# Kernel optimization log

Measured on AMD Instinct MI355X. Metric: run time of the kernel, lower is better.

## Reference

```python
import jax, jax.numpy as jnp
import numpy as np
from jax import lax

STRIDE = 8
DIST = float(np.sqrt(2.0) / 2.0)


def _conv_bn_leaky(x, w, gamma, beta):
    # 3x3 conv, stride 1, pad 1 (SAME), then batch-norm (training-mode batch stats) + leaky relu 0.1
    y = lax.conv_general_dilated(x, w, (1, 1), 'SAME',
                                 dimension_numbers=('NCHW', 'OIHW', 'NCHW'))
    m = y.mean(axis=(0, 2, 3))
    v = y.var(axis=(0, 2, 3))
    scale = (gamma / jnp.sqrt(v + 1e-5))[None, :, None, None]
    y = (y - m[None, :, None, None]) * scale + beta[None, :, None, None]
    return jnp.where(y > 0, y, 0.1 * y)


def _decode(p, offset_vertex):
    # p: [B,S,S,10], offset_vertex: [B,S,S,22]
    B, S = p.shape[0], p.shape[1]
    st = jnp.asarray(STRIDE, p.dtype)
    gx = jnp.tile(jnp.arange(S, dtype=p.dtype)[None, :], (S, 1))  # x varies along last dim
    gy = gx.T
    gX = gx[None, :, :, None]  # [1,S,S,1]
    gY = gy[None, :, :, None]

    raw_l, raw_s, raw_r, raw_conf = p[..., 0:4], p[..., 4:8], p[..., 8:9], p[..., 9:10]
    l = raw_l ** 2 * st
    xmin = gX * st + st / 2 - l[..., 3:4]
    ymin = gY * st + st / 2 - l[..., 0:1]
    xmax = gX * st + st / 2 + l[..., 1:2]
    ymax = gY * st + st / 2 + l[..., 2:3]
    w = l[..., 1:2] + l[..., 3:4]
    h = l[..., 0:1] + l[..., 2:3]
    xc = (xmax + xmin) / 2
    yc = (ymax + ymin) / 2
    xywh = jnp.concatenate([xc, yc, w, h], axis=-1)

    r = jax.nn.sigmoid(raw_r)
    maskr = jnp.where(r > 0.9, jnp.zeros_like(r), jnp.ones_like(r))
    s = jax.nn.sigmoid(raw_s) * maskr
    conf = jax.nn.sigmoid(raw_conf)
    bbox = jnp.concatenate([xywh, s, r, l, conf], axis=-1)  # [B,S,S,14]

    x1 = xmin + s[..., 0:1] * w
    x7 = xmax - s[..., 2:3] * w
    y5 = ymin + s[..., 1:2] * h
    y3 = ymax - s[..., 3:4] * h
    x_obb = (x1 + x7) / 2
    y_obb = (y5 + y3) / 2

    off_y_t = ymin / st + 1 - gY
    off_y_b = ymax / st - 1 - gY
    off_x_l = xmin / st + 1 - gX
    off_x_r = xmax / st - 1 - gX
    off_y3 = y3 / st - gY
    off_y4 = jnp.zeros_like(y_obb)
    off_y5 = y5 / st - gY
    off_x1 = x1 / st - gX
    off_x4 = jnp.zeros_like(x_obb)
    off_x7 = x7 / st - gX

    off = jax.nn.sigmoid(offset_vertex)
    dc_off = off[..., 4:]  # 18 channels
    eps = jnp.ceil(0.01 * w)

    xp0 = jnp.where(x1 < xmin + eps, x1, xmin + off[..., 0:1] * (x1 - xmin))
    yp0 = jnp.where(x1 < xmin + eps, ymin + off[..., 0:1] * (y3 - ymin),
                    (y3 - ymin) / (xmin - x1 + 1e-8) * (xp0 - x1) + ymin)
    xp2 = jnp.where(x1 > xmax - eps, x1, xmax - off[..., 1:2] * (xmax - x1))
    yp2 = jnp.where(x1 > xmax - eps, ymin + off[..., 1:2] * (y5 - ymin),
                    (y5 - ymin) / (xmax - x1 + 1e-8) * (xp2 - x1) + ymin)
    xp6 = jnp.where(x7 < xmin + eps, x7, xmin + off[..., 2:3] * (x7 - xmin))
    yp6 = jnp.where(x7 < xmin + eps, ymax - off[..., 2:3] * (ymax - y3),
                    (y3 - ymax) / (xmin - x7 + 1e-8) * (xp6 - x7) + ymax)
    xp8 = jnp.where(x7 > xmax - eps, x7, xmax - off[..., 3:4] * (xmax - x7))
    yp8 = jnp.where(x7 > xmax - eps, ymax - off[..., 3:4] * (ymax - y5),
                    (y5 - ymax) / (xmax - x7 + 1e-8) * (xp8 - x7) + ymax)

    off_y_0 = yp0 / st + 1 - gY
    off_x_0 = xp0 / st + 1 - gX
    off_y_2 = yp2 / st + 1 - gY
    off_x_2 = xp2 / st - 1 - gX
    off_y_6 = yp6 / st - 1 - gY
    off_x_6 = xp6 / st + 1 - gX
    off_y_8 = yp8 / st - 1 - gY
    off_x_8 = xp8 / st - 1 - gX

    offsets_loc = jnp.concatenate(
        [off_y_0, off_x_0, off_y_t, off_x1, off_y_2, off_x_2, off_y3, off_x_l,
         off_y4, off_x4, off_y5, off_x_r, off_y_6, off_x_6, off_y_b, off_x7,
         off_y_8, off_x_8], axis=-1)
    offsets_loc = jnp.transpose(offsets_loc, (0, 3, 1, 2))  # [B,18,S,S]

    width = lax.stop_gradient(jnp.sqrt((x1 - xmax) ** 2 + (ymin - y5) ** 2)
                              + jnp.sqrt((xmin - x7) ** 2 + (y3 - ymax) ** 2)) / 2
    height = lax.stop_gradient(jnp.sqrt((xmin - x1) ** 2 + (y3 - ymin) ** 2)
                               + jnp.sqrt((x7 - xmax) ** 2 + (ymax - y5) ** 2)) / 2
    angle = (jnp.arctan((y5 - ymin) / (xmax - x1 + 1e-4))
             + jnp.arctan((ymax - y3) / (x7 - xmin + 1e-4))) / 2

    xd = lax.stop_gradient(x_obb) - width / 2 + dc_off[..., 9:18] * width   # [B,S,S,9]
    yd = lax.stop_gradient(y_obb) - height / 2 + dc_off[..., 0:9] * height  # [B,S,S,9]
    ca, sa = jnp.cos(angle), jnp.sin(angle)
    xd0 = ca * (xd - x_obb) - sa * (yd - y_obb) + x_obb
    # faithful to the nested torch.where (outer branch uses the unclipped xd0)
    xd_ = jnp.where(jnp.where(xd0 >= xmin, xd0, xmin) <= xmax, xd0, xmax)
    yd0 = sa * (xd - x_obb) + ca * (yd - y_obb) + y_obb
    yd_ = jnp.where(jnp.where(yd0 >= ymin, yd0, ymin) <= ymax, yd0, ymax)

    dy = jnp.array([DIST, 1.0, DIST, 0.0, 0.0, 0.0, -DIST, -1.0, -DIST], p.dtype)
    dx = jnp.array([DIST, 0.0, -DIST, 1.0, 0.0, -1.0, DIST, 0.0, -DIST], p.dtype)
    dc_y = yd_ / st + dy - gY  # [B,S,S,9]
    dc_x = xd_ / st + dx - gX
    # interleave y0,x0,y1,x1,... -> 18 channels
    offsets_cls = jnp.stack([dc_y, dc_x], axis=-1).reshape(B, S, S, 18)
    offsets_cls = jnp.transpose(offsets_cls, (0, 3, 1, 2))

    coor_dc = jnp.concatenate([xd_, yd_], axis=-1).reshape(-1, 18)
    return bbox, offsets_loc, offsets_cls, coor_dc


def reference(input1, w_conv, bn_gamma, bn_beta, w_loc, b_loc, w_mask, b_mask):
    B, C, S, _ = input1.shape
    gx = jnp.tile(jnp.arange(S, dtype=input1.dtype)[None, :], (S, 1))
    gy = gx.T
    grid = jnp.broadcast_to(jnp.stack([gx, gy])[None], (B, 2, S, S))  # channel0=x, channel1=y
    x = jnp.concatenate([input1, grid], axis=1)
    conv = _conv_bn_leaky(x, w_conv, bn_gamma, bn_beta)  # [B, 2C, S, S]

    out1 = jnp.einsum('bchw,oc->bohw', conv, w_loc) + b_loc[None, :, None, None]
    cm = jnp.einsum('bchw,oc->bohw', conv, w_mask) + b_mask[None, :, None, None]

    mask_loc = jax.nn.sigmoid(cm[:, 0:9])
    mask_cls = jax.nn.sigmoid(cm[:, 9:18])
    offset_vertex = jnp.transpose(cm[:, 18:40], (0, 2, 3, 1))  # [B,S,S,22]
    weight_c8 = jax.nn.softmax(cm[:, 40:48], axis=1)

    p = jnp.transpose(out1, (0, 2, 3, 1))  # [B,S,S,10]
    bbox, offsets_loc, offsets_cls, offsets_d = _decode(p, offset_vertex)
    return (p, bbox, offsets_loc, offsets_cls, mask_loc, mask_cls, weight_c8, offsets_d)


def setup_inputs() -> dict:
    key = jax.random.key(0)
    ks = jax.random.split(key, 5)
    B, C, S = 16, 256, 64
    return {
        'input1': jax.random.normal(ks[0], (B, C, S, S), dtype=jnp.float32),
        'w_conv': jax.random.normal(ks[1], (2 * C, C + 2, 3, 3), dtype=jnp.float32) * 0.02,
        'bn_gamma': jnp.ones((2 * C,), jnp.float32),
        'bn_beta': jnp.zeros((2 * C,), jnp.float32),
        'w_loc': jax.random.normal(ks[2], (10, 2 * C), dtype=jnp.float32) * 0.02,
        'b_loc': jnp.zeros((10,), jnp.float32),
        'w_mask': jax.random.normal(ks[3], (48, 2 * C), dtype=jnp.float32) * 0.02,
        'b_mask': jnp.zeros((48,), jnp.float32),
    }
```

## Files before the change

### kernel.cpp

```cpp
#include <hip/hip_runtime.h>

typedef __attribute__((ext_vector_type(4))) float f32x4;
typedef __attribute__((ext_vector_type(4))) unsigned int u32x4;
typedef __attribute__((ext_vector_type(8))) unsigned short u16x8;
typedef __attribute__((ext_vector_type(8))) __bf16 bf16x8;

#define DEVFN static __device__ __forceinline__

DEVFN unsigned short f2b(float f) {
  unsigned u = __builtin_bit_cast(unsigned, f);
  u += 0x7fffu + ((u >> 16) & 1u);
  return (unsigned short)(u >> 16);
}
DEVFN float b2f(unsigned short h) {
  unsigned u = ((unsigned)h) << 16;
  return __builtin_bit_cast(float, u);
}
DEVFN float sigf(float x) { return 1.0f / (1.0f + __expf(-x)); }

#define CS 264
#define KPAD 2432
#define NTILE 38

#define XP_BYTES (16ull*66*66*CS*2)
#define WT_BYTES (512ull*KPAD*2)
#define W2_BYTES (64ull*512*2)
#define CV_BYTES (65536ull*512*2)
#define PS_BYTES (512ull*256*2*4)
#define XP_OFF 0ull
#define WT_OFF (XP_OFF + XP_BYTES)
#define W2_OFF (WT_OFF + WT_BYTES)
#define CV_OFF (W2_OFF + W2_BYTES)
#define PS_OFF (CV_OFF + CV_BYTES)
#define SB_OFF (PS_OFF + PS_BYTES)

#define GLOAD16(gp, lp) __builtin_amdgcn_global_load_lds( \
    (__attribute__((address_space(1))) void*)(gp),        \
    (__attribute__((address_space(3))) void*)(lp), 16, 0, 0)

#define BAR()  do { __builtin_amdgcn_s_barrier(); __builtin_amdgcn_sched_barrier(0); } while (0)
#define WLG0() do { asm volatile("s_waitcnt lgkmcnt(0)" ::: "memory"); __builtin_amdgcn_sched_barrier(0); } while (0)

__global__ void k_prep(const float* __restrict__ wc, const float* __restrict__ wl,
                       const float* __restrict__ wm, unsigned short* __restrict__ xp,
                       unsigned short* __restrict__ wt, unsigned short* __restrict__ w2) {
  int bid = blockIdx.x, tid = threadIdx.x;
  if (bid < 537) {
    int idx = bid * 256 + tid;
    if (idx >= 137280) return;
    int cell_i = idx / 33, u = idx - cell_i * 33;
    int b = cell_i / 260, r = cell_i - b * 260;
    int y, x;
    if (r < 66) { y = 0; x = r; }
    else if (r < 132) { y = 65; x = r - 66; }
    else if (r < 196) { y = r - 131; x = 0; }
    else { y = r - 195; x = 65; }
    int cell = (b * 66 + y) * 66 + x;
    *(u32x4*)((unsigned char*)xp + (size_t)cell * (CS * 2) + u * 16) = (u32x4){0u, 0u, 0u, 0u};
  } else if (bid < 793) {
    int pid = (bid - 537) * 256 + tid;
    int b = pid >> 12, pi = pid & 4095, y = pi >> 6, x = pi & 63;
    u16x8 v0 = (u16x8){0, 0, 0, 0, 0, 0, 0, 0};
    v0[0] = f2b((float)x); v0[1] = f2b((float)y);
    *(u16x8*)(xp + ((size_t)((b * 66 + y + 1) * 66 + x + 1)) * CS + 256) = v0;
  } else if (bid < 5657) {
    int idx = (bid - 793) * 256 + tid;
    int o = idx / KPAD, k = idx - o * KPAD;
    int dy = k / 800, t = k - dy * 800;
    int dx = t / CS, ci = t - dx * CS;
    float v = (dy < 3 && dx < 3 && ci < 258) ? wc[(size_t)(o * 258 + ci) * 9 + dy * 3 + dx] : 0.f;
    wt[idx] = f2b(v);
  } else {
    int idx = (bid - 5657) * 256 + tid;
    int o = idx >> 9, k = idx & 511;
    float v = 0.f;
    if (o < 10) v = wl[o * 512 + k];
    else if (o < 58) v = wm[(o - 10) * 512 + k];
    w2[idx] = f2b(v);
  }
}

__global__ void k_pack_in(const float* __restrict__ in1, unsigned short* __restrict__ xp) {
  __shared__ float lt[32][65];
  int tid = threadIdx.x;
  int bid = blockIdx.x;
  int cg = bid & 7, y = (bid >> 3) & 63, b = bid >> 9;
  int x = tid & 63, cr = tid >> 6;
#pragma unroll
  for (int i = 0; i < 8; ++i) {
    int cl = i * 4 + cr;
    lt[cl][x] = in1[(((size_t)(b * 256 + cg * 32 + cl) * 64 + y) * 64) + x];
  }
  __syncthreads();
  int xx = tid >> 2, ch = tid & 3;
  u16x8 v;
#pragma unroll
  for (int j = 0; j < 8; ++j) v[j] = f2b(lt[ch * 8 + j][xx]);
  size_t base = ((size_t)((b * 66 + y + 1) * 66 + xx + 1)) * CS + cg * 32 + ch * 8;
  *(u16x8*)(xp + base) = v;
}

__global__ __launch_bounds__(512, 2) void k_conv8(const unsigned short* __restrict__ xp,
                                                  const unsigned short* __restrict__ wt,
                                                  unsigned short* __restrict__ cv,
                                                  float* __restrict__ ps) {
  extern __shared__ char smem[];
  int tid = threadIdx.x, lane = tid & 63, wv = tid >> 6;
  int wm = wv >> 2, wn = wv & 3;
  int bid = blockIdx.x;
  int xcd = bid & 7, j = bid >> 3;
  int nt = j & 1;
  int mt = xcd * 32 + (j >> 1);
  int n0 = nt * 256;
  int pix0 = mt * 256;
  int b = pix0 >> 12, pi0 = pix0 & 4095;

  int srow = tid >> 3;
  int ug = (tid & 7) ^ (srow & 7);
  unsigned cellB[4], oB[4];
#pragma unroll
  for (int jj = 0; jj < 4; ++jj) {
    int pi = pi0 + srow + 64 * jj;
    int yy = pi >> 6, xx = pi & 63;
    cellB[jj] = (unsigned)((b * 66 + yy) * 66 + xx) * (CS * 2);
    oB[jj] = (unsigned)(n0 + srow + 64 * jj) * (KPAD * 2);
  }

  auto stageA = [&](int tau, int h) {
    int buf = tau & 1;
    unsigned k = (unsigned)tau * 64u + (unsigned)ug * 8u;
    unsigned dy = k / 800u;
    unsigned t = k - dy * 800u;
    unsigned off = dy * (66u * CS * 2u) + t * 2u;
    const unsigned char* g = (const unsigned char*)xp;
    char* l = smem + buf * 65536 + h * 16384;
    GLOAD16(g + cellB[h * 2] + off, l + tid * 16);
    GLOAD16(g + cellB[h * 2 + 1] + off, l + 8192 + tid * 16);
  };
  auto stageB = [&](int tau, int h) {
    int buf = tau & 1;
    unsigned k2 = ((unsigned)tau * 64u + (unsigned)ug * 8u) * 2u;
    const unsigned char* g = (const unsigned char*)wt;
    char* l = smem + buf * 65536 + 32768 + h * 16384;
    GLOAD16(g + oB[h * 2] + k2, l + tid * 16);
    GLOAD16(g + oB[h * 2 + 1] + k2, l + 8192 + tid * 16);
  };

  unsigned aoffb[8], boffb[4];
#pragma unroll
  for (int mf = 0; mf < 8; ++mf) aoffb[mf] = (unsigned)(wm * 128 + mf * 16 + (lane & 15)) * 128u;
#pragma unroll
  for (int nf = 0; nf < 4; ++nf) boffb[nf] = 32768u + (unsigned)(wn * 64 + nf * 16 + (lane & 15)) * 128u;
  int ko = (lane >> 4) & 3, xm = lane & 7;
  unsigned un[2];
#pragma unroll
  for (int kk = 0; kk < 2; ++kk) un[kk] = (unsigned)(((kk * 4 + ko) ^ xm) * 16);

  f32x4 acc[8][4];
#pragma unroll
  for (int i = 0; i < 8; ++i)
#pragma unroll
    for (int jj = 0; jj < 4; ++jj) acc[i][jj] = (f32x4){0.f, 0.f, 0.f, 0.f};

  stageB(0, 0); stageB(0, 1); stageA(0, 0); stageA(0, 1); stageB(1, 0); stageB(1, 1);
  asm volatile("s_waitcnt vmcnt(4)" ::: "memory");
  __builtin_amdgcn_sched_barrier(0);
  BAR();

  bf16x8 af[4][2], bfr[4][2];
#define MM(mi, ni, kk, ab) acc[(ab) + (mi)][(ni)] = \
    __builtin_amdgcn_mfma_f32_16x16x32_bf16(af[(mi)][(kk)], bfr[(ni)][(kk)], acc[(ab) + (mi)][(ni)], 0, 0, 0)

#pragma unroll 1
  for (int tau = 0; tau < NTILE; ++tau) {
    bool sA = tau < NTILE - 1, sB = tau < NTILE - 2;
    const char* base = smem + (tau & 1) * 65536;
    auto rdA = [&](int s, int kk, int hi) { af[s][kk] = *(const bf16x8*)(base + aoffb[hi * 4 + s] + un[kk]); };
    auto rdB = [&](int s, int kk) { bfr[s][kk] = *(const bf16x8*)(base + boffb[s] + un[kk]); };

    rdA(0, 0, 0); rdA(1, 0, 0); rdA(2, 0, 0); rdA(3, 0, 0);
    rdB(0, 0); rdB(1, 0); rdB(2, 0); rdB(3, 0);
    WLG0();
    __builtin_amdgcn_s_setprio(1);
    MM(0, 0, 0, 0); MM(0, 1, 0, 0); rdA(0, 1, 0);
    MM(0, 2, 0, 0); MM(0, 3, 0, 0); rdA(1, 1, 0);
    MM(1, 0, 0, 0); MM(1, 1, 0, 0); rdA(2, 1, 0);
    MM(1, 2, 0, 0); MM(1, 3, 0, 0); rdA(3, 1, 0);
    MM(2, 0, 0, 0); MM(2, 1, 0, 0); rdB(0, 1);
    MM(2, 2, 0, 0); MM(2, 3, 0, 0); rdB(1, 1);
    MM(3, 0, 0, 0); MM(3, 1, 0, 0); rdB(2, 1);
    MM(3, 2, 0, 0); MM(3, 3, 0, 0); rdB(3, 1);
    __builtin_amdgcn_s_setprio(0);
    if (sA) stageA(tau + 1, 0);
    BAR();

    WLG0();
    __builtin_amdgcn_s_setprio(1);
    MM(0, 0, 1, 0); MM(0, 1, 1, 0); MM(0, 2, 1, 0); MM(0, 3, 1, 0); rdA(0, 0, 1);
    MM(1, 0, 1, 0); MM(1, 1, 1, 0); MM(1, 2, 1, 0); MM(1, 3, 1, 0); rdA(1, 0, 1);
    MM(2, 0, 1, 0); MM(2, 1, 1, 0); MM(2, 2, 1, 0); MM(2, 3, 1, 0); rdA(2, 0, 1);
    MM(3, 0, 1, 0); MM(3, 1, 1, 0); MM(3, 2, 1, 0); MM(3, 3, 1, 0); rdA(3, 0, 1);
    __builtin_amdgcn_s_setprio(0);
    if (sA) stageA(tau + 1, 1);
    BAR();

    WLG0();
    __builtin_amdgcn_s_setprio(1);
    MM(0, 0, 0, 4); MM(0, 1, 0, 4); MM(0, 2, 0, 4); MM(0, 3, 0, 4); rdA(0, 1, 1);
    MM(1, 0, 0, 4); MM(1, 1, 0, 4); MM(1, 2, 0, 4); MM(1, 3, 0, 4); rdA(1, 1, 1);
    MM(2, 0, 0, 4); MM(2, 1, 0, 4); MM(2, 2, 0, 4); MM(2, 3, 0, 4); rdA(2, 1, 1);
    MM(3, 0, 0, 4); MM(3, 1, 0, 4); MM(3, 2, 0, 4); MM(3, 3, 0, 4); rdA(3, 1, 1);
    __builtin_amdgcn_s_setprio(0);
    if (sB) stageB(tau + 2, 0);
    BAR();

    WLG0();
    __builtin_amdgcn_s_setprio(1);
    MM(0, 0, 1, 4); MM(0, 1, 1, 4); MM(0, 2, 1, 4); MM(0, 3, 1, 4);
    MM(1, 0, 1, 4); MM(1, 1, 1, 4); MM(1, 2, 1, 4); MM(1, 3, 1, 4);
    MM(2, 0, 1, 4); MM(2, 1, 1, 4); MM(2, 2, 1, 4); MM(2, 3, 1, 4);
    MM(3, 0, 1, 4); MM(3, 1, 1, 4); MM(3, 2, 1, 4); MM(3, 3, 1, 4);
    __builtin_amdgcn_s_setprio(0);
    if (sB) stageB(tau + 2, 1);
    if (tau < NTILE - 2) { asm volatile("s_waitcnt vmcnt(4)" ::: "memory"); __builtin_amdgcn_sched_barrier(0); }
    else if (tau == NTILE - 2) { asm volatile("s_waitcnt vmcnt(0)" ::: "memory"); __builtin_amdgcn_sched_barrier(0); }
    BAR();
  }
#undef MM

  unsigned short* l16 = (unsigned short*)smem;
#pragma unroll
  for (int mf = 0; mf < 8; ++mf)
#pragma unroll
    for (int nf = 0; nf < 4; ++nf)
#pragma unroll
      for (int r = 0; r < 4; ++r) {
        int row = wm * 128 + mf * 16 + (lane >> 4) * 4 + r;
        int col = wn * 64 + nf * 16 + (lane & 15);
        int colx = col ^ (((row >> 2) & 3) << 3);
        l16[row * 256 + colx] = f2b(acc[mf][nf][r]);
      }
  __syncthreads();
#pragma unroll
  for (int i = 0; i < 16; ++i) {
    int q = tid + 512 * i;
    int prow = q >> 5, c16 = q & 31;
    int c16g = c16 ^ ((prow >> 2) & 3);
    *(u16x8*)(cv + ((size_t)(pix0 + prow) * 512 + n0 + c16g * 8)) = *(const u16x8*)(l16 + q * 8);
  }
  __syncthreads();

  float* lf = (float*)smem;
  float sv[4], qv[4];
#pragma unroll
  for (int nf = 0; nf < 4; ++nf) {
    float s = 0.f, q = 0.f;
#pragma unroll
    for (int mf = 0; mf < 8; ++mf)
#pragma unroll
      for (int r = 0; r < 4; ++r) { float v = acc[mf][nf][r]; s += v; q += v * v; }
    s += __shfl_xor(s, 16); s += __shfl_xor(s, 32);
    q += __shfl_xor(q, 16); q += __shfl_xor(q, 32);
    sv[nf] = s; qv[nf] = q;
  }
  if (lane < 16) {
#pragma unroll
    for (int nf = 0; nf < 4; ++nf) {
      int ch = wn * 64 + nf * 16 + lane;
      lf[wm * 256 + ch] = sv[nf];
      lf[512 + wm * 256 + ch] = qv[nf];
    }
  }
  __syncthreads();
  if (tid < 256) {
    float S = lf[tid] + lf[256 + tid];
    float Q = lf[512 + tid] + lf[768 + tid];
    ((float2*)ps)[(size_t)(n0 + tid) * 256 + mt] = make_float2(S, Q);
  }
}

__global__ void k_bnfinal(const float* __restrict__ ps, const float* __restrict__ gamma,
                          const float* __restrict__ beta, float* __restrict__ sb) {
  int c = blockIdx.x * 32 + (threadIdx.x >> 3);
  int sl = threadIdx.x & 7;
  const float2* p2 = (const float2*)ps + (size_t)c * 256 + sl * 32;
  float s = 0.f, q = 0.f;
#pragma unroll 8
  for (int i = 0; i < 32; ++i) { float2 v = p2[i]; s += v.x; q += v.y; }
  s += __shfl_xor(s, 1); s += __shfl_xor(s, 2); s += __shfl_xor(s, 4);
  q += __shfl_xor(q, 1); q += __shfl_xor(q, 2); q += __shfl_xor(q, 4);
  if (sl == 0) {
    float mean = s * (1.0f / 65536.0f);
    float var = q * (1.0f / 65536.0f) - mean * mean;
    float sc = gamma[c] / sqrtf(var + 1e-5f);
    sb[c] = sc;
    sb[512 + c] = beta[c] - mean * sc;
  }
}

__global__ __launch_bounds__(256) void k_head(const unsigned short* __restrict__ cv,
                                              const unsigned short* __restrict__ w2,
                                              const float* __restrict__ bl,
                                              const float* __restrict__ bm,
                                              const float* __restrict__ sb,
                                              float* __restrict__ out) {
  __shared__ float lo[256][59];
  __shared__ float sS[512], sBb[512];
  int tid = threadIdx.x, lane = tid & 63, wv = tid >> 6;
  int pix0 = blockIdx.x * 256;
  sS[tid] = sb[tid]; sS[256 + tid] = sb[256 + tid];
  sBb[tid] = sb[512 + tid]; sBb[256 + tid] = sb[768 + tid];
  __syncthreads();

  f32x4 acc[4][4];
#pragma unroll
  for (int mf = 0; mf < 4; ++mf)
#pragma unroll
    for (int nf = 0; nf < 4; ++nf) acc[mf][nf] = (f32x4){0.f, 0.f, 0.f, 0.f};
  int ko = lane >> 4;

  for (int k0 = 0; k0 < 512; k0 += 32) {
    int c0 = k0 + ko * 8;
    f32x4 sc0 = *(const f32x4*)&sS[c0], sc1 = *(const f32x4*)&sS[c0 + 4];
    f32x4 bo0 = *(const f32x4*)&sBb[c0], bo1 = *(const f32x4*)&sBb[c0 + 4];
    bf16x8 a[4], bg[4];
#pragma unroll
    for (int f = 0; f < 4; ++f) {
      bg[f] = *(const bf16x8*)(w2 + (size_t)(f * 16 + (lane & 15)) * 512 + c0);
      u16x8 raw = *(const u16x8*)(cv + (size_t)(pix0 + wv * 64 + f * 16 + (lane & 15)) * 512 + c0);
      u16x8 av;
#pragma unroll
      for (int jj = 0; jj < 4; ++jj) {
        float v = b2f(raw[jj]) * sc0[jj] + bo0[jj];
        v = (v > 0.f) ? v : 0.1f * v;
        av[jj] = f2b(v);
      }
#pragma unroll
      for (int jj = 0; jj < 4; ++jj) {
        float v = b2f(raw[4 + jj]) * sc1[jj] + bo1[jj];
        v = (v > 0.f) ? v : 0.1f * v;
        av[4 + jj] = f2b(v);
      }
      a[f] = __builtin_bit_cast(bf16x8, av);
    }
#pragma unroll
    for (int mf = 0; mf < 4; ++mf)
#pragma unroll
      for (int nf = 0; nf < 4; ++nf)
        acc[mf][nf] = __builtin_amdgcn_mfma_f32_16x16x32_bf16(a[mf], bg[nf], acc[mf][nf], 0, 0, 0);
  }

  float bias[4]; int colv[4];
#pragma unroll
  for (int nf = 0; nf < 4; ++nf) {
    int col = nf * 16 + (lane & 15);
    colv[nf] = col;
    bias[nf] = (col < 10) ? bl[col] : ((col < 58) ? bm[col - 10] : 0.f);
  }
#pragma unroll
  for (int mf = 0; mf < 4; ++mf)
#pragma unroll
    for (int nf = 0; nf < 4; ++nf)
#pragma unroll
      for (int r = 0; r < 4; ++r) {
        int row = wv * 64 + mf * 16 + (lane >> 4) * 4 + r;
        if (colv[nf] < 58) lo[row][colv[nf]] = acc[mf][nf][r] + bias[nf];
      }
  __syncthreads();

  int pix = pix0 + tid;
  int b = pix >> 12, pi = pix & 4095;
  int yi = pi >> 6, xi = pi & 63;
  float X = (float)xi, Y = (float)yi;
  const float* O = lo[tid];

  float* outP = out;
  float* outB = out + 655360;
  float* outOL = out + 1572864;
  float* outOC = out + 2752512;
  float* outML = out + 3932160;
  float* outMC = out + 4521984;
  float* outWC = out + 5111808;
  float* outOD = out + 5636096;

  float pr[10];
#pragma unroll
  for (int i = 0; i < 10; ++i) { pr[i] = O[i]; outP[(size_t)pix * 10 + i] = pr[i]; }
  const float st = 8.f, ist = 0.125f;
  float l0 = pr[0] * pr[0] * st, l1 = pr[1] * pr[1] * st;
  float l2 = pr[2] * pr[2] * st, l3 = pr[3] * pr[3] * st;
  float cx = X * st + 4.f, cy = Y * st + 4.f;
  float xmin = cx - l3, ymin = cy - l0, xmax = cx + l1, ymax = cy + l2;
  float w = l1 + l3, h = l0 + l2;
  float xc = 0.5f * (xmax + xmin), yc = 0.5f * (ymax + ymin);
  float r = sigf(pr[8]);
  float maskr = (r > 0.9f) ? 0.f : 1.f;
  float s0 = sigf(pr[4]) * maskr, s1 = sigf(pr[5]) * maskr;
  float s2 = sigf(pr[6]) * maskr, s3 = sigf(pr[7]) * maskr;
  float conf = sigf(pr[9]);
  {
    size_t bo = (size_t)pix * 14;
    outB[bo + 0] = xc; outB[bo + 1] = yc; outB[bo + 2] = w; outB[bo + 3] = h;
    outB[bo + 4] = s0; outB[bo + 5] = s1; outB[bo + 6] = s2; outB[bo + 7] = s3;
    outB[bo + 8] = r;  outB[bo + 9] = l0; outB[bo + 10] = l1; outB[bo + 11] = l2;
    outB[bo + 12] = l3; outB[bo + 13] = conf;
  }
  float x1 = xmin + s0 * w, x7 = xmax - s2 * w;
  float y5 = ymin + s1 * h, y3 = ymax - s3 * h;
  float xob = 0.5f * (x1 + x7), yob = 0.5f * (y5 + y3);
  float ov[22];
#pragma unroll
  for (int jj = 0; jj < 22; ++jj) ov[jj] = sigf(O[28 + jj]);
  float eps = ceilf(0.01f * w);
  bool c0 = x1 < xmin + eps;
  float xp0 = c0 ? x1 : xmin + ov[0] * (x1 - xmin);
  float yp0 = c0 ? ymin + ov[0] * (y3 - ymin)
                 : (y3 - ymin) / (xmin - x1 + 1e-8f) * (xp0 - x1) + ymin;
  bool c2 = x1 > xmax - eps;
  float xp2 = c2 ? x1 : xmax - ov[1] * (xmax - x1);
  float yp2 = c2 ? ymin + ov[1] * (y5 - ymin)
                 : (y5 - ymin) / (xmax - x1 + 1e-8f) * (xp2 - x1) + ymin;
  bool c6 = x7 < xmin + eps;
  float xp6 = c6 ? x7 : xmin + ov[2] * (x7 - xmin);
  float yp6 = c6 ? ymax - ov[2] * (ymax - y3)
                 : (y3 - ymax) / (xmin - x7 + 1e-8f) * (xp6 - x7) + ymax;
  bool c8c = x7 > xmax - eps;
  float xp8 = c8c ? x7 : xmax - ov[3] * (xmax - x7);
  float yp8 = c8c ? ymax - ov[3] * (ymax - y5)
                  : (y5 - ymax) / (xmax - x7 + 1e-8f) * (xp8 - x7) + ymax;

  size_t olb = ((size_t)b * 18) * 4096 + pi;
  outOL[olb + 0 * 4096] = yp0 * ist + 1.f - Y;
  outOL[olb + 1 * 4096] = xp0 * ist + 1.f - X;
  outOL[olb + 2 * 4096] = ymin * ist + 1.f - Y;
  outOL[olb + 3 * 4096] = x1 * ist - X;
  outOL[olb + 4 * 4096] = yp2 * ist + 1.f - Y;
  outOL[olb + 5 * 4096] = xp2 * ist - 1.f - X;
  outOL[olb + 6 * 4096] = y3 * ist - Y;
  outOL[olb + 7 * 4096] = xmin * ist + 1.f - X;
  outOL[olb + 8 * 4096] = 0.f;
  outOL[olb + 9 * 4096] = 0.f;
  outOL[olb + 10 * 4096] = y5 * ist - Y;
  outOL[olb + 11 * 4096] = xmax * ist - 1.f - X;
  outOL[olb + 12 * 4096] = yp6 * ist - 1.f - Y;
  outOL[olb + 13 * 4096] = xp6 * ist + 1.f - X;
  outOL[olb + 14 * 4096] = ymax * ist - 1.f - Y;
  outOL[olb + 15 * 4096] = x7 * ist - X;
  outOL[olb + 16 * 4096] = yp8 * ist - 1.f - Y;
  outOL[olb + 17 * 4096] = xp8 * ist - 1.f - X;

  float A1 = x1 - xmax, B1 = ymin - y5, A2 = xmin - x7, B2 = y3 - ymax;
  float width = 0.5f * (sqrtf(A1 * A1 + B1 * B1) + sqrtf(A2 * A2 + B2 * B2));
  float C1 = xmin - x1, D1 = y3 - ymin, C2 = x7 - xmax, D2 = ymax - y5;
  float height = 0.5f * (sqrtf(C1 * C1 + D1 * D1) + sqrtf(C2 * C2 + D2 * D2));
  float ang = 0.5f * (atanf((y5 - ymin) / (xmax - x1 + 1e-4f)) +
                      atanf((ymax - y3) / (x7 - xmin + 1e-4f)));
  float ca = cosf(ang), sa = sinf(ang);
  const float DD = 0.70710678118654752f;
  const float dyc[9] = {DD, 1.f, DD, 0.f, 0.f, 0.f, -DD, -1.f, -DD};
  const float dxc[9] = {DD, 0.f, -DD, 1.f, 0.f, -1.f, DD, 0.f, -DD};
  size_t ocb = ((size_t)b * 18) * 4096 + pi;
  size_t odb = (size_t)pix * 18;
#pragma unroll
  for (int k = 0; k < 9; ++k) {
    float xd = xob - 0.5f * width + ov[13 + k] * width;
    float yd = yob - 0.5f * height + ov[4 + k] * height;
    float ddx = xd - xob, ddy = yd - yob;
    float xd0 = ca * ddx - sa * ddy + xob;
    float xdc = fminf(fmaxf(xd0, xmin), xmax);
    float yd0 = sa * ddx + ca * ddy + yob;
    float ydc = fminf(fmaxf(yd0, ymin), ymax);
    outOC[ocb + (size_t)(2 * k) * 4096] = ydc * ist + dyc[k] - Y;
    outOC[ocb + (size_t)(2 * k + 1) * 4096] = xdc * ist + dxc[k] - X;
    outOD[odb + k] = xdc;
    outOD[odb + 9 + k] = ydc;
  }
  size_t mlb = ((size_t)b * 9) * 4096 + pi;
#pragma unroll
  for (int k = 0; k < 9; ++k) outML[mlb + (size_t)k * 4096] = sigf(O[10 + k]);
#pragma unroll
  for (int k = 0; k < 9; ++k) outMC[mlb + (size_t)k * 4096] = sigf(O[19 + k]);
  float v8[8], mx = -1e30f;
#pragma unroll
  for (int k = 0; k < 8; ++k) { v8[k] = O[50 + k]; mx = fmaxf(mx, v8[k]); }
  float sm = 0.f;
#pragma unroll
  for (int k = 0; k < 8; ++k) { v8[k] = __expf(v8[k] - mx); sm += v8[k]; }
  float inv = 1.f / sm;
  size_t wcb = ((size_t)b * 8) * 4096 + pi;
#pragma unroll
  for (int k = 0; k < 8; ++k) outWC[wcb + (size_t)k * 4096] = v8[k] * inv;
}

extern "C" void kernel_launch(void* const* d_in, const int* in_sizes, int n_in,
                              void* d_out, int out_size, void* d_ws, size_t ws_size,
                              hipStream_t stream) {
  const float* in1 = (const float*)d_in[0];
  const float* wconv = (const float*)d_in[1];
  const float* gamma = (const float*)d_in[2];
  const float* beta = (const float*)d_in[3];
  const float* wloc = (const float*)d_in[4];
  const float* bloc = (const float*)d_in[5];
  const float* wmask = (const float*)d_in[6];
  const float* bmask = (const float*)d_in[7];
  unsigned char* ws = (unsigned char*)d_ws;
  unsigned short* xp = (unsigned short*)(ws + XP_OFF);
  unsigned short* wt = (unsigned short*)(ws + WT_OFF);
  unsigned short* w2 = (unsigned short*)(ws + W2_OFF);
  unsigned short* cv = (unsigned short*)(ws + CV_OFF);
  float* ps = (float*)(ws + PS_OFF);
  float* sb = (float*)(ws + SB_OFF);
  float* out = (float*)d_out;

  (void)hipFuncSetAttribute(reinterpret_cast<const void*>(k_conv8),
                            hipFuncAttributeMaxDynamicSharedMemorySize, 131072);

  k_prep<<<dim3(5785), dim3(256), 0, stream>>>(wconv, wloc, wmask, xp, wt, w2);
  k_pack_in<<<dim3(8192), dim3(256), 0, stream>>>(in1, xp);
  k_conv8<<<dim3(512), dim3(512), 131072, stream>>>(xp, wt, cv, ps);
  k_bnfinal<<<dim3(16), dim3(256), 0, stream>>>(ps, gamma, beta, sb);
  k_head<<<dim3(256), dim3(256), 0, stream>>>(cv, w2, bloc, bmask, sb, out);
}
```

Baseline: 211.6 us.

## Load conv weight fragments directly to registers from pre-swizzled global layout

The prep kernel now writes the conv weights in a fragment-ordered layout, so each lane can load its MFMA B operands straight from global memory into registers. The weights are double-buffered in registers one tile ahead, which removes weight staging through LDS and halves LDS use per stage. The main loop is restructured to have one barrier per K-tile instead of four. In exchange, every wave fetches its own weight fragments from global or L2 memory, register pressure rises, and each tile waits on vmcnt(0).

```diff
diff --git a/kernel.cpp b/kernel.cpp
--- a/kernel.cpp
+++ b/kernel.cpp
@@ -43,7 +43,7 @@
 
 __global__ void k_prep(const float* __restrict__ wc, const float* __restrict__ wl,
                        const float* __restrict__ wm, unsigned short* __restrict__ xp,
-                       unsigned short* __restrict__ wt, unsigned short* __restrict__ w2) {
+                       unsigned short* __restrict__ wt2, unsigned short* __restrict__ w2) {
   int bid = blockIdx.x, tid = threadIdx.x;
   if (bid < 537) {
     int idx = bid * 256 + tid;
@@ -69,7 +69,10 @@
     int dy = k / 800, t = k - dy * 800;
     int dx = t / CS, ci = t - dx * CS;
     float v = (dy < 3 && dx < 3 && ci < 258) ? wc[(size_t)(o * 258 + ci) * 9 + dy * 3 + dx] : 0.f;
-    wt[idx] = f2b(v);
+    int ntv = o >> 8, o2 = o & 255, wn = o2 >> 6, o3 = o2 & 63, nf = o3 >> 4, r = o3 & 15;
+    int tau = k >> 6, k2 = k & 63, kk = k2 >> 5, k3 = k2 & 31, ko = k3 >> 3, e = k3 & 7;
+    size_t off = ((size_t)(((ntv * 38 + tau) * 4 + wn) * 8 + nf * 2 + kk)) * 512 + (ko * 16 + r) * 8 + e;
+    wt2[off] = f2b(v);
   } else {
     int idx = (bid - 5657) * 256 + tid;
     int o = idx >> 9, k = idx & 511;
@@ -101,7 +104,7 @@
 }
 
 __global__ __launch_bounds__(512, 2) void k_conv8(const unsigned short* __restrict__ xp,
-                                                  const unsigned short* __restrict__ wt,
+                                                  const unsigned short* __restrict__ wt2,
                                                   unsigned short* __restrict__ cv,
                                                   float* __restrict__ ps) {
   extern __shared__ char smem[];
@@ -117,13 +120,12 @@
 
   int srow = tid >> 3;
   int ug = (tid & 7) ^ (srow & 7);
-  unsigned cellB[4], oB[4];
+  unsigned cellB[4];
 #pragma unroll
   for (int jj = 0; jj < 4; ++jj) {
     int pi = pi0 + srow + 64 * jj;
     int yy = pi >> 6, xx = pi & 63;
     cellB[jj] = (unsigned)((b * 66 + yy) * 66 + xx) * (CS * 2);
-    oB[jj] = (unsigned)(n0 + srow + 64 * jj) * (KPAD * 2);
   }
 
   auto stageA = [&](int tau, int h) {
@@ -133,100 +135,163 @@
     unsigned t = k - dy * 800u;
     unsigned off = dy * (66u * CS * 2u) + t * 2u;
     const unsigned char* g = (const unsigned char*)xp;
-    char* l = smem + buf * 65536 + h * 16384;
+    char* l = smem + buf * 32768 + h * 16384;
     GLOAD16(g + cellB[h * 2] + off, l + tid * 16);
     GLOAD16(g + cellB[h * 2 + 1] + off, l + 8192 + tid * 16);
   };
-  auto stageB = [&](int tau, int h) {
-    int buf = tau & 1;
-    unsigned k2 = ((unsigned)tau * 64u + (unsigned)ug * 8u) * 2u;
-    const unsigned char* g = (const unsigned char*)wt;
-    char* l = smem + buf * 65536 + 32768 + h * 16384;
-    GLOAD16(g + oB[h * 2] + k2, l + tid * 16);
-    GLOAD16(g + oB[h * 2 + 1] + k2, l + 8192 + tid * 16);
-  };
-
-  unsigned aoffb[8], boffb[4];
+
+  unsigned aoffb[8];
 #pragma unroll
   for (int mf = 0; mf < 8; ++mf) aoffb[mf] = (unsigned)(wm * 128 + mf * 16 + (lane & 15)) * 128u;
-#pragma unroll
-  for (int nf = 0; nf < 4; ++nf) boffb[nf] = 32768u + (unsigned)(wn * 64 + nf * 16 + (lane & 15)) * 128u;
   int ko = (lane >> 4) & 3, xm = lane & 7;
   unsigned un[2];
 #pragma unroll
   for (int kk = 0; kk < 2; ++kk) un[kk] = (unsigned)(((kk * 4 + ko) ^ xm) * 16);
 
+  const char* wb = (const char*)wt2 + ((size_t)(nt * 38 * 4 + wn) * 8) * 1024 + (size_t)lane * 16;
+  const size_t WTAU = 4 * 8 * 1024;
+
   f32x4 acc[8][4];
 #pragma unroll
   for (int i = 0; i < 8; ++i)
 #pragma unroll
     for (int jj = 0; jj < 4; ++jj) acc[i][jj] = (f32x4){0.f, 0.f, 0.f, 0.f};
 
-  stageB(0, 0); stageB(0, 1); stageA(0, 0); stageA(0, 1); stageB(1, 0); stageB(1, 1);
-  asm volatile("s_waitcnt vmcnt(4)" ::: "memory");
+  bf16x8 af[4][2], bA[4][2], bB[4][2];
+
+  stageA(0, 0); stageA(0, 1);
+#pragma unroll
+  for (int nf = 0; nf < 4; ++nf) {
+    bA[nf][0] = *(const bf16x8*)(wb + (nf * 2 + 0) * 1024);
+    bA[nf][1] = *(const bf16x8*)(wb + (nf * 2 + 1) * 1024);
+  }
+  asm volatile("s_waitcnt vmcnt(0)" ::: "memory");
   __builtin_amdgcn_sched_barrier(0);
   BAR();
-
-  bf16x8 af[4][2], bfr[4][2];
-#define MM(mi, ni, kk, ab) acc[(ab) + (mi)][(ni)] = \
-    __builtin_amdgcn_mfma_f32_16x16x32_bf16(af[(mi)][(kk)], bfr[(ni)][(kk)], acc[(ab) + (mi)][(ni)], 0, 0, 0)
+  {
+    const char* base0 = smem;
+#pragma unroll
+    for (int s = 0; s < 4; ++s) af[s][0] = *(const bf16x8*)(base0 + aoffb[s] + un[0]);
+  }
+
+#define MMX(mi, ni, kk, ab, BC) acc[(ab) + (mi)][(ni)] = \
+    __builtin_amdgcn_mfma_f32_16x16x32_bf16(af[(mi)][(kk)], BC[(ni)][(kk)], acc[(ab) + (mi)][(ni)], 0, 0, 0)
+
+#define TILE_STEADY(tau, BC, BN)                                                        \
+  {                                                                                     \
+    const char* base = smem + ((tau) & 1) * 32768;                                      \
+    const char* nbase = smem + (((tau) + 1) & 1) * 32768;                               \
+    const char* wbn = wb + (size_t)((tau) + 1) * WTAU;                                  \
+                                                                    \
+    BN[0][0] = *(const bf16x8*)(wbn + 0 * 1024);                                        \
+    BN[0][1] = *(const bf16x8*)(wbn + 1 * 1024);                                        \
+    BN[1][0] = *(const bf16x8*)(wbn + 2 * 1024);                                        \
+    BN[1][1] = *(const bf16x8*)(wbn + 3 * 1024);                                        \
+    BN[2][0] = *(const bf16x8*)(wbn + 4 * 1024);                                        \
+    BN[2][1] = *(const bf16x8*)(wbn + 5 * 1024);                                        \
+    BN[3][0] = *(const bf16x8*)(wbn + 6 * 1024);                                        \
+    BN[3][1] = *(const bf16x8*)(wbn + 7 * 1024);                                        \
+                                                        \
+    WLG0();                                                                             \
+    __builtin_amdgcn_s_setprio(1);                                                      \
+    MMX(0, 0, 0, 0, BC); MMX(0, 1, 0, 0, BC); MMX(0, 2, 0, 0, BC); MMX(0, 3, 0, 0, BC); \
+    af[0][1] = *(const bf16x8*)(base + aoffb[0] + un[1]);                               \
+    MMX(1, 0, 0, 0, BC); MMX(1, 1, 0, 0, BC); MMX(1, 2, 0, 0, BC); MMX(1, 3, 0, 0, BC); \
+    af[1][1] = *(const bf16x8*)(base + aoffb[1] + un[1]);                               \
+    MMX(2, 0, 0, 0, BC); MMX(2, 1, 0, 0, BC); MMX(2, 2, 0, 0, BC); MMX(2, 3, 0, 0, BC); \
+    af[2][1] = *(const bf16x8*)(base + aoffb[2] + un[1]);                               \
+    MMX(3, 0, 0, 0, BC); MMX(3, 1, 0, 0, BC); MMX(3, 2, 0, 0, BC); MMX(3, 3, 0, 0, BC); \
+    af[3][1] = *(const bf16x8*)(base + aoffb[3] + un[1]);                               \
+    __builtin_amdgcn_s_setprio(0);                                                      \
+    stageA((tau) + 1, 0);                                                               \
+                                                        \
+    WLG0();                                                                             \
+    __builtin_amdgcn_s_setprio(1);                                                      \
+    MMX(0, 0, 1, 0, BC); MMX(0, 1, 1, 0, BC); MMX(0, 2, 1, 0, BC); MMX(0, 3, 1, 0, BC); \
+    af[0][0] = *(const bf16x8*)(base + aoffb[4] + un[0]);                               \
+    MMX(1, 0, 1, 0, BC); MMX(1, 1, 1, 0, BC); MMX(1, 2, 1, 0, BC); MMX(1, 3, 1, 0, BC); \
+    af[1][0] = *(const bf16x8*)(base + aoffb[5] + un[0]);                               \
+    MMX(2, 0, 1, 0, BC); MMX(2, 1, 1, 0, BC); MMX(2, 2, 1, 0, BC); MMX(2, 3, 1, 0, BC); \
+    af[2][0] = *(const bf16x8*)(base + aoffb[6] + un[0]);                               \
+    MMX(3, 0, 1, 0, BC); MMX(3, 1, 1, 0, BC); MMX(3, 2, 1, 0, BC); MMX(3, 3, 1, 0, BC); \
+    af[3][0] = *(const bf16x8*)(base + aoffb[7] + un[0]);                               \
+    __builtin_amdgcn_s_setprio(0);                                                      \
+    stageA((tau) + 1, 1);                                                               \
+                         \
+    WLG0();                                                                             \
+    __builtin_amdgcn_s_setprio(1);                                                      \
+    MMX(0, 0, 0, 4, BC); MMX(0, 1, 0, 4, BC); MMX(0, 2, 0, 4, BC); MMX(0, 3, 0, 4, BC); \
+    af[0][1] = *(const bf16x8*)(base + aoffb[4] + un[1]);                               \
+    MMX(1, 0, 0, 4, BC); MMX(1, 1, 0, 4, BC); MMX(1, 2, 0, 4, BC); MMX(1, 3, 0, 4, BC); \
+    af[1][1] = *(const bf16x8*)(base + aoffb[5] + un[1]);                               \
+    MMX(2, 0, 0, 4, BC); MMX(2, 1, 0, 4, BC); MMX(2, 2, 0, 4, BC); MMX(2, 3, 0, 4, BC); \
+    af[2][1] = *(const bf16x8*)(base + aoffb[6] + un[1]);                               \
+    MMX(3, 0, 0, 4, BC); MMX(3, 1, 0, 4, BC); MMX(3, 2, 0, 4, BC); MMX(3, 3, 0, 4, BC); \
+    af[3][1] = *(const bf16x8*)(base + aoffb[7] + un[1]);                               \
+    __builtin_amdgcn_s_setprio(0);                                                      \
+    asm volatile("s_waitcnt vmcnt(0) lgkmcnt(0)" ::: "memory");                         \
+    __builtin_amdgcn_sched_barrier(0);                                                  \
+    BAR();                                                                              \
+                                                   \
+    __builtin_amdgcn_s_setprio(1);                                                      \
+    MMX(0, 0, 1, 4, BC); MMX(0, 1, 1, 4, BC); MMX(0, 2, 1, 4, BC); MMX(0, 3, 1, 4, BC); \
+    af[0][0] = *(const bf16x8*)(nbase + aoffb[0] + un[0]);                              \
+    MMX(1, 0, 1, 4, BC); MMX(1, 1, 1, 4, BC); MMX(1, 2, 1, 4, BC); MMX(1, 3, 1, 4, BC); \
+    af[1][0] = *(const bf16x8*)(nbase + aoffb[1] + un[0]);                              \
+    MMX(2, 0, 1, 4, BC); MMX(2, 1, 1, 4, BC); MMX(2, 2, 1, 4, BC); MMX(2, 3, 1, 4, BC); \
+    af[2][0] = *(const bf16x8*)(nbase + aoffb[2] + un[0]);                              \
+    MMX(3, 0, 1, 4, BC); MMX(3, 1, 1, 4, BC); MMX(3, 2, 1, 4, BC); MMX(3, 3, 1, 4, BC); \
+    af[3][0] = *(const bf16x8*)(nbase + aoffb[3] + un[0]);                              \
+    __builtin_amdgcn_s_setprio(0);                                                      \
+  }
 
 #pragma unroll 1
-  for (int tau = 0; tau < NTILE; ++tau) {
-    bool sA = tau < NTILE - 1, sB = tau < NTILE - 2;
-    const char* base = smem + (tau & 1) * 65536;
-    auto rdA = [&](int s, int kk, int hi) { af[s][kk] = *(const bf16x8*)(base + aoffb[hi * 4 + s] + un[kk]); };
-    auto rdB = [&](int s, int kk) { bfr[s][kk] = *(const bf16x8*)(base + boffb[s] + un[kk]); };
-
-    rdA(0, 0, 0); rdA(1, 0, 0); rdA(2, 0, 0); rdA(3, 0, 0);
-    rdB(0, 0); rdB(1, 0); rdB(2, 0); rdB(3, 0);
+  for (int t2 = 0; t2 < 18; ++t2) {
+    int tau = t2 * 2;
+    TILE_STEADY(tau, bA, bB);
+    TILE_STEADY(tau + 1, bB, bA);
+  }
+  TILE_STEADY(36, bA, bB);
+
+  {
+    const char* base = smem + 32768;
     WLG0();
-    __builtin_amdgcn_s_setprio(1);
-    MM(0, 0, 0, 0); MM(0, 1, 0, 0); rdA(0, 1, 0);
-    MM(0, 2, 0, 0); MM(0, 3, 0, 0); rdA(1, 1, 0);
-    MM(1, 0, 0, 0); MM(1, 1, 0, 0); rdA(2, 1, 0);
-    MM(1, 2, 0, 0); MM(1, 3, 0, 0); rdA(3, 1, 0);
-    MM(2, 0, 0, 0); MM(2, 1, 0, 0); rdB(0, 1);
-    MM(2, 2, 0, 0); MM(2, 3, 0, 0); rdB(1, 1);
-    MM(3, 0, 0, 0); MM(3, 1, 0, 0); rdB(2, 1);
-    MM(3, 2, 0, 0); MM(3, 3, 0, 0); rdB(3, 1);
-    __builtin_amdgcn_s_setprio(0);
-    if (sA) stageA(tau + 1, 0);
-    BAR();
-
+    MMX(0, 0, 0, 0, bB); MMX(0, 1, 0, 0, bB); MMX(0, 2, 0, 0, bB); MMX(0, 3, 0, 0, bB);
+    af[0][1] = *(const bf16x8*)(base + aoffb[0] + un[1]);
+    MMX(1, 0, 0, 0, bB); MMX(1, 1, 0, 0, bB); MMX(1, 2, 0, 0, bB); MMX(1, 3, 0, 0, bB);
+    af[1][1] = *(const bf16x8*)(base + aoffb[1] + un[1]);
+    MMX(2, 0, 0, 0, bB); MMX(2, 1, 0, 0, bB); MMX(2, 2, 0, 0, bB); MMX(2, 3, 0, 0, bB);
+    af[2][1] = *(const bf16x8*)(base + aoffb[2] + un[1]);
+    MMX(3, 0, 0, 0, bB); MMX(3, 1, 0, 0, bB); MMX(3, 2, 0, 0, bB); MMX(3, 3, 0, 0, bB);
+    af[3][1] = *(const bf16x8*)(base + aoffb[3] + un[1]);
     WLG0();
-    __builtin_amdgcn_s_setprio(1);
-    MM(0, 0, 1, 0); MM(0, 1, 1, 0); MM(0, 2, 1, 0); MM(0, 3, 1, 0); rdA(0, 0, 1);
-    MM(1, 0, 1, 0); MM(1, 1, 1, 0); MM(1, 2, 1, 0); MM(1, 3, 1, 0); rdA(1, 0, 1);
-    MM(2, 0, 1, 0); MM(2, 1, 1, 0); MM(2, 2, 1, 0); MM(2, 3, 1, 0); rdA(2, 0, 1);
-    MM(3, 0, 1, 0); MM(3, 1, 1, 0); MM(3, 2, 1, 0); MM(3, 3, 1, 0); rdA(3, 0, 1);
-    __builtin_amdgcn_s_setprio(0);
-    if (sA) stageA(tau + 1, 1);
-    BAR();
-
+    MMX(0, 0, 1, 0, bB); MMX(0, 1, 1, 0, bB); MMX(0, 2, 1, 0, bB); MMX(0, 3, 1, 0, bB);
+    af[0][0] = *(const bf16x8*)(base + aoffb[4] + un[0]);
+    MMX(1, 0, 1, 0, bB); MMX(1, 1, 1, 0, bB); MMX(1, 2, 1, 0, bB); MMX(1, 3, 1, 0, bB);
+    af[1][0] = *(const bf16x8*)(base + aoffb[5] + un[0]);
+    MMX(2, 0, 1, 0, bB); MMX(2, 1, 1, 0, bB); MMX(2, 2, 1, 0, bB); MMX(2, 3, 1, 0, bB);
+    af[2][0] = *(const bf16x8*)(base + aoffb[6] + un[0]);
+    MMX(3, 0, 1, 0, bB); MMX(3, 1, 1, 0, bB); MMX(3, 2, 1, 0, bB); MMX(3, 3, 1, 0, bB);
+    af[3][0] = *(const bf16x8*)(base + aoffb[7] + un[0]);
     WLG0();
-    __builtin_amdgcn_s_setprio(1);
-    MM(0, 0, 0, 4); MM(0, 1, 0, 4); MM(0, 2, 0, 4); MM(0, 3, 0, 4); rdA(0, 1, 1);
-    MM(1, 0, 0, 4); MM(1, 1, 0, 4); MM(1, 2, 0, 4); MM(1, 3, 0, 4); rdA(1, 1, 1);
-    MM(2, 0, 0, 4); MM(2, 1, 0, 4); MM(2, 2, 0, 4); MM(2, 3, 0, 4); rdA(2, 1, 1);
-    MM(3, 0, 0, 4); MM(3, 1, 0, 4); MM(3, 2, 0, 4); MM(3, 3, 0, 4); rdA(3, 1, 1);
-    __builtin_amdgcn_s_setprio(0);
-    if (sB) stageB(tau + 2, 0);
-    BAR();
-
+    MMX(0, 0, 0, 4, bB); MMX(0, 1, 0, 4, bB); MMX(0, 2, 0, 4, bB); MMX(0, 3, 0, 4, bB);
+    af[0][1] = *(const bf16x8*)(base + aoffb[4] + un[1]);
+    MMX(1, 0, 0, 4, bB); MMX(1, 1, 0, 4, bB); MMX(1, 2, 0, 4, bB); MMX(1, 3, 0, 4, bB);
+    af[1][1] = *(const bf16x8*)(base + aoffb[5] + un[1]);
+    MMX(2, 0, 0, 4, bB); MMX(2, 1, 0, 4, bB); MMX(2, 2, 0, 4, bB); MMX(2, 3, 0, 4, bB);
+    af[2][1] = *(const bf16x8*)(base + aoffb[6] + un[1]);
+    MMX(3, 0, 0, 4, bB); MMX(3, 1, 0, 4, bB); MMX(3, 2, 0, 4, bB); MMX(3, 3, 0, 4, bB);
+    af[3][1] = *(const bf16x8*)(base + aoffb[7] + un[1]);
     WLG0();
-    __builtin_amdgcn_s_setprio(1);
-    MM(0, 0, 1, 4); MM(0, 1, 1, 4); MM(0, 2, 1, 4); MM(0, 3, 1, 4);
-    MM(1, 0, 1, 4); MM(1, 1, 1, 4); MM(1, 2, 1, 4); MM(1, 3, 1, 4);
-    MM(2, 0, 1, 4); MM(2, 1, 1, 4); MM(2, 2, 1, 4); MM(2, 3, 1, 4);
-    MM(3, 0, 1, 4); MM(3, 1, 1, 4); MM(3, 2, 1, 4); MM(3, 3, 1, 4);
-    __builtin_amdgcn_s_setprio(0);
-    if (sB) stageB(tau + 2, 1);
-    if (tau < NTILE - 2) { asm volatile("s_waitcnt vmcnt(4)" ::: "memory"); __builtin_amdgcn_sched_barrier(0); }
-    else if (tau == NTILE - 2) { asm volatile("s_waitcnt vmcnt(0)" ::: "memory"); __builtin_amdgcn_sched_barrier(0); }
-    BAR();
-  }
-#undef MM
+    MMX(0, 0, 1, 4, bB); MMX(0, 1, 1, 4, bB); MMX(0, 2, 1, 4, bB); MMX(0, 3, 1, 4, bB);
+    MMX(1, 0, 1, 4, bB); MMX(1, 1, 1, 4, bB); MMX(1, 2, 1, 4, bB); MMX(1, 3, 1, 4, bB);
+    MMX(2, 0, 1, 4, bB); MMX(2, 1, 1, 4, bB); MMX(2, 2, 1, 4, bB); MMX(2, 3, 1, 4, bB);
+    MMX(3, 0, 1, 4, bB); MMX(3, 1, 1, 4, bB); MMX(3, 2, 1, 4, bB); MMX(3, 3, 1, 4, bB);
+  }
+#undef MMX
+#undef TILE_STEADY
+
+  __syncthreads();
 
   unsigned short* l16 = (unsigned short*)smem;
 #pragma unroll
@@ -505,7 +570,7 @@
   const float* bmask = (const float*)d_in[7];
   unsigned char* ws = (unsigned char*)d_ws;
   unsigned short* xp = (unsigned short*)(ws + XP_OFF);
-  unsigned short* wt = (unsigned short*)(ws + WT_OFF);
+  unsigned short* wt2 = (unsigned short*)(ws + WT_OFF);
   unsigned short* w2 = (unsigned short*)(ws + W2_OFF);
   unsigned short* cv = (unsigned short*)(ws + CV_OFF);
   float* ps = (float*)(ws + PS_OFF);
@@ -515,9 +580,9 @@
   (void)hipFuncSetAttribute(reinterpret_cast<const void*>(k_conv8),
                             hipFuncAttributeMaxDynamicSharedMemorySize, 131072);
 
-  k_prep<<<dim3(5785), dim3(256), 0, stream>>>(wconv, wloc, wmask, xp, wt, w2);
+  k_prep<<<dim3(5785), dim3(256), 0, stream>>>(wconv, wloc, wmask, xp, wt2, w2);
   k_pack_in<<<dim3(8192), dim3(256), 0, stream>>>(in1, xp);
-  k_conv8<<<dim3(512), dim3(512), 131072, stream>>>(xp, wt, cv, ps);
+  k_conv8<<<dim3(512), dim3(512), 131072, stream>>>(xp, wt2, cv, ps);
   k_bnfinal<<<dim3(16), dim3(256), 0, stream>>>(ps, gamma, beta, sb);
   k_head<<<dim3(256), dim3(256), 0, stream>>>(cv, w2, bloc, bmask, sb, out);
 }
```

After: 213.7 us. About the same (+1.0%).
